# Performance work log

Measured on AMD Instinct MI355X. Metric: run time of the kernel, lower is better.

## Reference

```python
import jax, jax.numpy as jnp
import numpy as np

B, T_IN, T_OUT = 512, 256, 128
V, N, EH, DH, SD = 256, 1024, 64, 128, 32


def _lstm_scan(gx_seq, W_hh, h0, c0):
    """gx_seq: (T, B, 4H) precomputed input-side gates (incl. bias).
    PyTorch LSTMCell gate order: i, f, g, o."""
    def step(carry, gx):
        h, c = carry
        g = gx + h @ W_hh.T                       # (B, 4H)
        i, f, gg, o = jnp.split(g, 4, axis=-1)
        c2 = jax.nn.sigmoid(f) * c + jax.nn.sigmoid(i) * jnp.tanh(gg)
        h2 = jax.nn.sigmoid(o) * jnp.tanh(c2)
        return (h2, c2), h2
    (hT, cT), hs = jax.lax.scan(step, (h0, c0), gx_seq)
    return hT, hs


def _forward(inp_onehot, zia, tgt, fortza,
             enc_Wih, enc_Whh, enc_b, sg_W, sg_b,
             Wc_W, Wc_b, dec_Wih, dec_Whh, dec_b, out_W, out_b):
    Bb = inp_onehot.shape[0]
    dt = inp_onehot.dtype
    # ---- encoder: input projection hoisted out of the recurrence ----
    # enc_in = concat([x_t, zia]); zia is constant over t, so its gate
    # contribution is computed once (same math as the per-step cat+GEMM).
    Wx, Wz = enc_Wih[:, :V], enc_Wih[:, V:]          # (4EH,V), (4EH,N)
    gx_const = zia @ Wz.T + enc_b                    # (B, 4EH)
    gx_enc = jnp.einsum('btv,gv->tbg', inp_onehot, Wx) + gx_const[None]
    h0 = jnp.zeros((Bb, EH), dt)
    h_enc, _ = _lstm_scan(gx_enc, enc_Whh, h0, h0)   # (B, EH)
    # ---- soul update ----
    sg = jnp.concatenate([h_enc, fortza], axis=-1) @ sg_W.T + sg_b
    gate = jax.nn.sigmoid(sg[:, :SD])
    update = jnp.tanh(sg[:, SD:])
    fortza_new = gate * fortza + (1.0 - gate) * update
    # ---- decoder init ----
    dh0 = jnp.tanh(jnp.concatenate([h_enc, zia], axis=-1) @ Wc_W.T + Wc_b)
    dc0 = jnp.zeros_like(dh0)
    # ---- decoder recurrence ----
    gx_dec = jnp.einsum('btv,gv->tbg', tgt, dec_Wih) + dec_b
    _, dhs = _lstm_scan(gx_dec, dec_Whh, dh0, dc0)   # (T_out, B, DH)
    # ---- output projection: split cat([dh, fortza_new]) @ W.T ----
    Wd, Wf = out_W[:, :DH], out_W[:, DH:]
    logits = (jnp.einsum('tbh,vh->btv', dhs, Wd)
              + (fortza_new @ Wf.T)[:, None, :] + out_b)
    return logits, fortza_new


def setup_inputs() -> dict:
    key = jax.random.key(0)
    ks = jax.random.split(key, 20)
    f32 = jnp.float32
    def nrm(k, shape, s=0.05):
        return jax.random.normal(k, shape, f32) * s
    inp_idx = jax.random.randint(ks[0], (B, T_IN), 0, V)
    tgt_idx = jax.random.randint(ks[1], (B, T_OUT), 0, V)
    return {
        'inp_onehot': jax.nn.one_hot(inp_idx, V, dtype=f32),
        'zia': jax.random.uniform(ks[2], (B, N), f32),
        'tgt': jax.nn.one_hot(tgt_idx, V, dtype=f32),
        'fortza': nrm(ks[3], (B, SD), 0.5),
        'enc_Wih': nrm(ks[4], (4 * EH, V + N)),
        'enc_Whh': nrm(ks[5], (4 * EH, EH)),
        'enc_b': nrm(ks[6], (4 * EH,)),
        'sg_W': nrm(ks[7], (2 * SD, EH + SD)),
        'sg_b': nrm(ks[8], (2 * SD,)),
        'Wc_W': nrm(ks[9], (DH, EH + N)),
        'Wc_b': nrm(ks[10], (DH,)),
        'dec_Wih': nrm(ks[11], (4 * DH, V)),
        'dec_Whh': nrm(ks[12], (4 * DH, DH)),
        'dec_b': nrm(ks[13], (4 * DH,)),
        'out_W': nrm(ks[14], (V, DH + SD)),
        'out_b': nrm(ks[15], (V,)),
    }


def reference(inp_onehot, zia, tgt, fortza,
              enc_Wih, enc_Whh, enc_b, sg_W, sg_b,
              Wc_W, Wc_b, dec_Wih, dec_Whh, dec_b, out_W, out_b):
    return _forward(inp_onehot, zia, tgt, fortza,
                    enc_Wih, enc_Whh, enc_b, sg_W, sg_b,
                    Wc_W, Wc_b, dec_Wih, dec_Whh, dec_b, out_W, out_b)
```

## Files before the change

kernel.cpp:

```cpp
#include <hip/hip_runtime.h>
#include <hip/hip_bf16.h>

#define BATCH 512
#define TIN   256
#define TOUT  128
#define VOC   256
#define NZ    1024
#define EHID  64
#define DHID  128
#define SDIM  32

typedef __attribute__((ext_vector_type(8))) short bf16x8;
typedef __attribute__((ext_vector_type(4))) float f32x4;

__device__ __forceinline__ float bf2f(unsigned short u) {
  return __uint_as_float(((unsigned)u) << 16);
}
__device__ __forceinline__ unsigned short f2bf(float f) {
  unsigned u = __float_as_uint(f);
  u = u + 0x7FFFu + ((u >> 16) & 1u);
  return (unsigned short)(u >> 16);
}
__device__ __forceinline__ float sigf(float x) { return 1.0f / (1.0f + __expf(-x)); }
__device__ __forceinline__ float tanh_(float x) { return 1.0f - 2.0f / (1.0f + __expf(2.0f * x)); }

__device__ __forceinline__ bf16x8 pack8(float4 a, float4 b) {
  bf16x8 r;
  r[0] = (short)f2bf(a.x); r[1] = (short)f2bf(a.y);
  r[2] = (short)f2bf(a.z); r[3] = (short)f2bf(a.w);
  r[4] = (short)f2bf(b.x); r[5] = (short)f2bf(b.y);
  r[6] = (short)f2bf(b.z); r[7] = (short)f2bf(b.w);
  return r;
}

__global__ void k_prep(const float* __restrict__ enc_Wih, const float* __restrict__ enc_b,
                       const float* __restrict__ dec_Wih, const float* __restrict__ dec_b,
                       const float* __restrict__ out_W,
                       float* __restrict__ WxT, float* __restrict__ WdecT,
                       float* __restrict__ WdT) {
  int blk = blockIdx.x, tid = threadIdx.x;
  if (blk < 256) {
    if (tid < 256)
      WxT[blk * 256 + tid] = enc_Wih[(size_t)tid * (VOC + NZ) + blk] + enc_b[tid];
  } else if (blk < 512) {
    int v = blk - 256;
    WdecT[v * 512 + tid] = dec_Wih[(size_t)tid * VOC + v] + dec_b[tid];
  } else {
    int k = blk - 512;
    if (tid < 256)
      WdT[k * 256 + tid] = out_W[(size_t)tid * (DHID + SDIM) + k];
  }
}

__global__ void k_findidx(const float* __restrict__ src, int n_pos,
                          int* __restrict__ out) {
  int pos = blockIdx.x * 4 + (threadIdx.x >> 6);
  int lane = threadIdx.x & 63;
  if (pos >= n_pos) return;
  float4 v = ((const float4*)src)[(size_t)pos * 64 + lane];
  int comp = v.x > 0.5f ? 0 : (v.y > 0.5f ? 1 : (v.z > 0.5f ? 2 : 3));
  bool hit = (v.x > 0.5f) || (v.y > 0.5f) || (v.z > 0.5f) || (v.w > 0.5f);
  int cand = hit ? lane * 4 + comp : (1 << 30);
#pragma unroll
  for (int off = 32; off > 0; off >>= 1) {
    int o = __shfl_xor(cand, off);
    cand = cand < o ? cand : o;
  }
  if (lane == 0) out[pos] = cand < VOC ? cand : VOC - 1;
}

__global__ __launch_bounds__(256) void k_gx_const(
    const float* __restrict__ zia, const float* __restrict__ enc_Wih,
    float* __restrict__ gxc) {
  __shared__ float zs[NZ];
  int b = blockIdx.x, g = threadIdx.x;
  ((float4*)zs)[g] = ((const float4*)(zia + (size_t)b * NZ))[g];
  __syncthreads();
  float acc = 0.0f;
  const float4* wr = (const float4*)(enc_Wih + (size_t)g * (VOC + NZ) + VOC);
  const float4* z4 = (const float4*)zs;
#pragma unroll 8
  for (int k4 = 0; k4 < NZ / 4; ++k4) {
    float4 w = wr[k4], z = z4[k4];
    acc += w.x * z.x + w.y * z.y + w.z * z.z + w.w * z.w;
  }
  gxc[b * 256 + g] = acc;
}

#define ESTR 72
__global__ __launch_bounds__(256) void k_enc_scan_mfma(
    const float* __restrict__ enc_Whh, const float* __restrict__ WxT,
    const float* __restrict__ gxc, const int* __restrict__ enc_idx,
    float* __restrict__ h_enc) {
  __shared__ unsigned short hA[2][16 * ESTR];
  __shared__ int idx_s[4][TIN];
  int b0 = blockIdx.x * 4;
  int tid = threadIdx.x;
  int w = tid >> 6, lane = tid & 63, n = lane & 15, quad = lane >> 4;
  int j0 = w * 16, j = j0 + n;

  bf16x8 Bf[4][2];
#pragma unroll
  for (int ty = 0; ty < 4; ++ty)
#pragma unroll
    for (int kb = 0; kb < 2; ++kb) {
      const float* src = enc_Whh + (size_t)(ty * 64 + j0 + n) * EHID + kb * 32 + quad * 8;
      float4 x = *(const float4*)src, y = *(const float4*)(src + 4);
      Bf[ty][kb] = pack8(x, y);
    }
  for (int i = tid; i < 16 * ESTR; i += 256) { hA[0][i] = 0; hA[1][i] = 0; }
  for (int i = tid; i < 4 * TIN; i += 256)
    idx_s[i >> 8][i & 255] = enc_idx[(size_t)(b0 + (i >> 8)) * TIN + (i & 255)];
  float gc[4];
#pragma unroll
  for (int ty = 0; ty < 4; ++ty) gc[ty] = gxc[(size_t)(b0 + quad) * 256 + ty * 64 + j];
  __syncthreads();

  float gx[4];
  {
    int id0 = idx_s[quad][0];
#pragma unroll
    for (int ty = 0; ty < 4; ++ty) gx[ty] = WxT[(size_t)id0 * 256 + ty * 64 + j];
  }
  float c0 = 0.0f, h = 0.0f;
  for (int t = 0; t < TIN; ++t) {
    const unsigned short* cur = hA[t & 1];
    bf16x8 a[2];
#pragma unroll
    for (int kb = 0; kb < 2; ++kb)
      a[kb] = *(const bf16x8*)(cur + n * ESTR + kb * 32 + quad * 8);
    float gxn[4];
    int tn = (t + 1 < TIN) ? t + 1 : t;
    int idn = idx_s[quad][tn];
#pragma unroll
    for (int ty = 0; ty < 4; ++ty) gxn[ty] = WxT[(size_t)idn * 256 + ty * 64 + j];
    f32x4 acc[4];
#pragma unroll
    for (int ty = 0; ty < 4; ++ty) {
      f32x4 z; z[0] = gx[ty] + gc[ty]; z[1] = 0.f; z[2] = 0.f; z[3] = 0.f;
#pragma unroll
      for (int kb = 0; kb < 2; ++kb)
        z = __builtin_amdgcn_mfma_f32_16x16x32_bf16(a[kb], Bf[ty][kb], z, 0, 0, 0);
      acc[ty] = z;
    }
    float gi = acc[0][0], gf = acc[1][0], gg = acc[2][0], go = acc[3][0];
    c0 = sigf(gf) * c0 + sigf(gi) * tanh_(gg);
    h = sigf(go) * tanh_(c0);
    hA[(t + 1) & 1][(quad * 4) * ESTR + j] = f2bf(h);
    gx[0] = gxn[0]; gx[1] = gxn[1]; gx[2] = gxn[2]; gx[3] = gxn[3];
    __syncthreads();
  }
  h_enc[(size_t)(b0 + quad) * EHID + j] = h;
}

__global__ __launch_bounds__(256) void k_sg_fortza(
    const float* __restrict__ h_enc, const float* __restrict__ fortza,
    const float* __restrict__ sg_W, const float* __restrict__ sg_b,
    const float* __restrict__ out_W, const float* __restrict__ out_b,
    float* __restrict__ out_fortza, float* __restrict__ fout) {
  __shared__ float hf[EHID], fz[SDIM], sg_s[2 * SDIM], fn[SDIM];
  int b = blockIdx.x, tid = threadIdx.x;
  if (tid < EHID) hf[tid] = h_enc[b * EHID + tid];
  if (tid >= EHID && tid < EHID + SDIM)
    fz[tid - EHID] = fortza[(size_t)b * SDIM + (tid - EHID)];
  __syncthreads();
  if (tid < 2 * SDIM) {
    float acc = sg_b[tid];
    const float* row = sg_W + (size_t)tid * (EHID + SDIM);
    for (int k = 0; k < EHID; ++k) acc += hf[k] * row[k];
    for (int j = 0; j < SDIM; ++j) acc += fz[j] * row[EHID + j];
    sg_s[tid] = acc;
  }
  __syncthreads();
  if (tid < SDIM) {
    float gate = sigf(sg_s[tid]);
    float upd = tanh_(sg_s[SDIM + tid]);
    float v = gate * fz[tid] + (1.0f - gate) * upd;
    fn[tid] = v;
    out_fortza[(size_t)b * SDIM + tid] = v;
  }
  __syncthreads();
  {
    float acc = out_b[tid];
    const float* row = out_W + (size_t)tid * (DHID + SDIM) + DHID;
    for (int j = 0; j < SDIM; ++j) acc += fn[j] * row[j];
    fout[b * VOC + tid] = acc;
  }
}

__global__ __launch_bounds__(128) void k_dh0(
    const float* __restrict__ h_enc, const float* __restrict__ zia,
    const float* __restrict__ Wc_W, const float* __restrict__ Wc_b,
    float* __restrict__ dh0) {
  __shared__ float xs[EHID + NZ];
  int b = blockIdx.x, v = threadIdx.x;
  if (v < EHID) xs[v] = h_enc[b * EHID + v];
  for (int i = v; i < NZ / 4; i += 128)
    ((float4*)(xs + EHID))[i] = ((const float4*)(zia + (size_t)b * NZ))[i];
  __syncthreads();
  float acc = Wc_b[v];
  const float4* wr = (const float4*)(Wc_W + (size_t)v * (EHID + NZ));
  const float4* x4 = (const float4*)xs;
#pragma unroll 8
  for (int k4 = 0; k4 < (EHID + NZ) / 4; ++k4) {
    float4 w = wr[k4], x = x4[k4];
    acc += w.x * x.x + w.y * x.y + w.z * x.z + w.w * x.w;
  }
  dh0[b * DHID + v] = tanh_(acc);
}

#define DSTR 136
__global__ __launch_bounds__(512) void k_dec_scan_mfma(
    const float* __restrict__ dec_Whh, const float* __restrict__ WdecT,
    const int* __restrict__ dec_idx, const float* __restrict__ dh0,
    unsigned short* __restrict__ dhs) {
  __shared__ unsigned short hA[2][16 * DSTR];
  __shared__ int idx_s[4][TOUT];
  int b0 = blockIdx.x * 4;
  int tid = threadIdx.x;
  int w = tid >> 6, lane = tid & 63, n = lane & 15, quad = lane >> 4;
  int j0 = w * 16, j = j0 + n;

  bf16x8 Bf[4][4];
#pragma unroll
  for (int ty = 0; ty < 4; ++ty)
#pragma unroll
    for (int kb = 0; kb < 4; ++kb) {
      const float* src = dec_Whh + (size_t)(ty * 128 + j0 + n) * DHID + kb * 32 + quad * 8;
      float4 x = *(const float4*)src, y = *(const float4*)(src + 4);
      Bf[ty][kb] = pack8(x, y);
    }
  for (int i = tid; i < 16 * DSTR; i += 512) {
    int m = i / DSTR, k = i - m * DSTR;
    float v = (k < DHID && (m & 3) == 0) ? dh0[(size_t)(b0 + (m >> 2)) * DHID + k] : 0.0f;
    hA[0][i] = f2bf(v);
    hA[1][i] = 0;
  }
  for (int i = tid; i < 4 * TOUT; i += 512)
    idx_s[i >> 7][i & 127] = dec_idx[(size_t)(b0 + (i >> 7)) * TOUT + (i & 127)];
  __syncthreads();

  float gx[4];
  {
    int id0 = idx_s[quad][0];
#pragma unroll
    for (int ty = 0; ty < 4; ++ty) gx[ty] = WdecT[(size_t)id0 * 512 + ty * 128 + j];
  }
  float c0 = 0.0f;
  for (int t = 0; t < TOUT; ++t) {
    const unsigned short* cur = hA[t & 1];
    bf16x8 a[4];
#pragma unroll
    for (int kb = 0; kb < 4; ++kb)
      a[kb] = *(const bf16x8*)(cur + n * DSTR + kb * 32 + quad * 8);
    float gxn[4];
    int tn = (t + 1 < TOUT) ? t + 1 : t;
    int idn = idx_s[quad][tn];
#pragma unroll
    for (int ty = 0; ty < 4; ++ty) gxn[ty] = WdecT[(size_t)idn * 512 + ty * 128 + j];
    f32x4 acc[4];
#pragma unroll
    for (int ty = 0; ty < 4; ++ty) {
      f32x4 z; z[0] = gx[ty]; z[1] = 0.f; z[2] = 0.f; z[3] = 0.f;
#pragma unroll
      for (int kb = 0; kb < 4; ++kb)
        z = __builtin_amdgcn_mfma_f32_16x16x32_bf16(a[kb], Bf[ty][kb], z, 0, 0, 0);
      acc[ty] = z;
    }
    float gi = acc[0][0], gf = acc[1][0], gg = acc[2][0], go = acc[3][0];
    c0 = sigf(gf) * c0 + sigf(gi) * tanh_(gg);
    float h = sigf(go) * tanh_(c0);
    unsigned short hb = f2bf(h);
    hA[(t + 1) & 1][(quad * 4) * DSTR + j] = hb;
    dhs[((size_t)t * BATCH + b0 + quad) * DHID + j] = hb;
    gx[0] = gxn[0]; gx[1] = gxn[1]; gx[2] = gxn[2]; gx[3] = gxn[3];
    __syncthreads();
  }
}

__global__ __launch_bounds__(256) void k_logits(const unsigned short* __restrict__ dhs,
                                                const float* __restrict__ WdT,
                                                const float* __restrict__ fout,
                                                float* __restrict__ out) {
  __shared__ float s[DHID * 64];
  int r0 = blockIdx.x * 64;
  int t = r0 / BATCH;
  int b0 = r0 % BATCH;
  int tid = threadIdx.x;
  for (int i = tid; i < 64 * DHID; i += 256) {
    int m = i >> 7;
    int k = i & 127;
    s[k * 64 + m] = bf2f(dhs[(size_t)(r0 + m) * DHID + k]);
  }
  __syncthreads();
  int v4 = tid & 63;
  int mg = tid >> 6;
  float4 acc[16];
#pragma unroll
  for (int m = 0; m < 16; ++m) acc[m] = make_float4(0.f, 0.f, 0.f, 0.f);
  for (int k = 0; k < DHID; ++k) {
    float4 wv = ((const float4*)(WdT + k * 256))[v4];
    const float4* sk = (const float4*)(s + k * 64 + mg * 16);
#pragma unroll
    for (int j = 0; j < 4; ++j) {
      float4 h4 = sk[j];
      acc[j * 4 + 0].x += h4.x * wv.x; acc[j * 4 + 0].y += h4.x * wv.y;
      acc[j * 4 + 0].z += h4.x * wv.z; acc[j * 4 + 0].w += h4.x * wv.w;
      acc[j * 4 + 1].x += h4.y * wv.x; acc[j * 4 + 1].y += h4.y * wv.y;
      acc[j * 4 + 1].z += h4.y * wv.z; acc[j * 4 + 1].w += h4.y * wv.w;
      acc[j * 4 + 2].x += h4.z * wv.x; acc[j * 4 + 2].y += h4.z * wv.y;
      acc[j * 4 + 2].z += h4.z * wv.z; acc[j * 4 + 2].w += h4.z * wv.w;
      acc[j * 4 + 3].x += h4.w * wv.x; acc[j * 4 + 3].y += h4.w * wv.y;
      acc[j * 4 + 3].z += h4.w * wv.z; acc[j * 4 + 3].w += h4.w * wv.w;
    }
  }
#pragma unroll
  for (int m = 0; m < 16; ++m) {
    int bb = b0 + mg * 16 + m;
    float4 fo = ((const float4*)(fout + bb * VOC))[v4];
    float4 r;
    r.x = acc[m].x + fo.x;
    r.y = acc[m].y + fo.y;
    r.z = acc[m].z + fo.z;
    r.w = acc[m].w + fo.w;
    ((float4*)(out + ((size_t)bb * TOUT + t) * VOC))[v4] = r;
  }
}

extern "C" void kernel_launch(void* const* d_in, const int* in_sizes, int n_in,
                              void* d_out, int out_size, void* d_ws, size_t ws_size,
                              hipStream_t stream) {
  const float* inp_onehot = (const float*)d_in[0];
  const float* zia     = (const float*)d_in[1];
  const float* tgt     = (const float*)d_in[2];
  const float* fortza  = (const float*)d_in[3];
  const float* enc_Wih = (const float*)d_in[4];
  const float* enc_Whh = (const float*)d_in[5];
  const float* enc_b   = (const float*)d_in[6];
  const float* sg_W    = (const float*)d_in[7];
  const float* sg_b    = (const float*)d_in[8];
  const float* Wc_W    = (const float*)d_in[9];
  const float* Wc_b    = (const float*)d_in[10];
  const float* dec_Wih = (const float*)d_in[11];
  const float* dec_Whh = (const float*)d_in[12];
  const float* dec_b   = (const float*)d_in[13];
  const float* out_W   = (const float*)d_in[14];
  const float* out_b   = (const float*)d_in[15];
  float* out = (float*)d_out;

  float* ws = (float*)d_ws;
  int* enc_idx  = (int*)d_ws;
  int* dec_idx  = enc_idx + BATCH * TIN;
  float* WxT    = ws + 196608;
  float* WdecT  = ws + 262144;
  float* WdT    = ws + 393216;
  float* gxc    = ws + 425984;
  float* h_enc  = ws + 557056;
  float* dh0    = ws + 589824;
  float* fout   = ws + 655360;
  unsigned short* dhs = (unsigned short*)(ws + 786432);

  k_prep<<<640, 512, 0, stream>>>(enc_Wih, enc_b, dec_Wih, dec_b, out_W, WxT, WdecT, WdT);
  k_findidx<<<BATCH * TIN / 4, 256, 0, stream>>>(inp_onehot, BATCH * TIN, enc_idx);
  k_findidx<<<BATCH * TOUT / 4, 256, 0, stream>>>(tgt, BATCH * TOUT, dec_idx);
  k_gx_const<<<BATCH, 256, 0, stream>>>(zia, enc_Wih, gxc);
  k_enc_scan_mfma<<<BATCH / 4, 256, 0, stream>>>(enc_Whh, WxT, gxc, enc_idx, h_enc);
  k_sg_fortza<<<BATCH, 256, 0, stream>>>(h_enc, fortza, sg_W, sg_b, out_W, out_b,
                                         out + (size_t)BATCH * TOUT * VOC, fout);
  k_dh0<<<BATCH, 128, 0, stream>>>(h_enc, zia, Wc_W, Wc_b, dh0);
  k_dec_scan_mfma<<<BATCH / 4, 512, 0, stream>>>(dec_Whh, WdecT, dec_idx, dh0, dhs);
  k_logits<<<TOUT * BATCH / 64, 256, 0, stream>>>(dhs, WdT, fout, out);
}
```

Measured before the change: 629.5 us.

## Merge prep kernels and overlap decoder prep with encoder scan via block-role dispatch

Collapses nine launches into five by giving blocks of one launch different roles. The decoder weight transposes and target index extraction now run as extra blocks alongside the latency-bound encoder scan, so they can use otherwise idle CUs. The zia-side gate GEMM and the decoder init GEMM are rewritten as shared-memory tiled 32x32 GEMMs, and the weight transposes go through an LDS tile for coalesced access. The cost is a larger, more divergent kernel with heavier resource use, which could reduce occupancy of the scan blocks or delay their scheduling behind the auxiliary blocks.

Result: faster. 568.6 us (-9.7%).

```diff
diff --git a/kernel.cpp b/kernel.cpp
--- a/kernel.cpp
+++ b/kernel.cpp
@@ -33,30 +33,9 @@
   return r;
 }
 
-__global__ void k_prep(const float* __restrict__ enc_Wih, const float* __restrict__ enc_b,
-                       const float* __restrict__ dec_Wih, const float* __restrict__ dec_b,
-                       const float* __restrict__ out_W,
-                       float* __restrict__ WxT, float* __restrict__ WdecT,
-                       float* __restrict__ WdT) {
-  int blk = blockIdx.x, tid = threadIdx.x;
-  if (blk < 256) {
-    if (tid < 256)
-      WxT[blk * 256 + tid] = enc_Wih[(size_t)tid * (VOC + NZ) + blk] + enc_b[tid];
-  } else if (blk < 512) {
-    int v = blk - 256;
-    WdecT[v * 512 + tid] = dec_Wih[(size_t)tid * VOC + v] + dec_b[tid];
-  } else {
-    int k = blk - 512;
-    if (tid < 256)
-      WdT[k * 256 + tid] = out_W[(size_t)tid * (DHID + SDIM) + k];
-  }
-}
-
-__global__ void k_findidx(const float* __restrict__ src, int n_pos,
-                          int* __restrict__ out) {
-  int pos = blockIdx.x * 4 + (threadIdx.x >> 6);
-  int lane = threadIdx.x & 63;
-  if (pos >= n_pos) return;
+__device__ __forceinline__ void dev_findidx(const float* __restrict__ src,
+                                            int pos, int lane,
+                                            int* __restrict__ out) {
   float4 v = ((const float4*)src)[(size_t)pos * 64 + lane];
   int comp = v.x > 0.5f ? 0 : (v.y > 0.5f ? 1 : (v.z > 0.5f ? 2 : 3));
   bool hit = (v.x > 0.5f) || (v.y > 0.5f) || (v.z > 0.5f) || (v.w > 0.5f);
@@ -69,148 +48,218 @@
   if (lane == 0) out[pos] = cand < VOC ? cand : VOC - 1;
 }
 
-__global__ __launch_bounds__(256) void k_gx_const(
-    const float* __restrict__ zia, const float* __restrict__ enc_Wih,
-    float* __restrict__ gxc) {
-  __shared__ float zs[NZ];
-  int b = blockIdx.x, g = threadIdx.x;
-  ((float4*)zs)[g] = ((const float4*)(zia + (size_t)b * NZ))[g];
-  __syncthreads();
-  float acc = 0.0f;
-  const float4* wr = (const float4*)(enc_Wih + (size_t)g * (VOC + NZ) + VOC);
-  const float4* z4 = (const float4*)zs;
-#pragma unroll 8
-  for (int k4 = 0; k4 < NZ / 4; ++k4) {
-    float4 w = wr[k4], z = z4[k4];
-    acc += w.x * z.x + w.y * z.y + w.z * z.z + w.w * z.w;
-  }
-  gxc[b * 256 + g] = acc;
+__global__ __launch_bounds__(256) void k_pre(
+    const float* __restrict__ enc_Wih, const float* __restrict__ enc_b,
+    const float* __restrict__ inp_onehot, const float* __restrict__ zia,
+    float* __restrict__ WxT, float* __restrict__ gxc, int* __restrict__ enc_idx) {
+  int blk = blockIdx.x, tid = threadIdx.x;
+  if (blk < 64) {
+    __shared__ float T[32][36];
+    int r = tid >> 3, c = (tid & 7) * 4;
+    int g0 = (blk >> 3) * 32, v0 = (blk & 7) * 32;
+    float4 v = *(const float4*)(enc_Wih + (size_t)(g0 + r) * (VOC + NZ) + v0 + c);
+    float bias = enc_b[g0 + r];
+    T[c + 0][r] = v.x + bias; T[c + 1][r] = v.y + bias;
+    T[c + 2][r] = v.z + bias; T[c + 3][r] = v.w + bias;
+    __syncthreads();
+    *(float4*)(WxT + (size_t)(v0 + r) * 256 + g0 + c) = *(const float4*)&T[r][c];
+  } else if (blk < 192) {
+    __shared__ float As[32][36], Bs[32][36];
+    int q = blk - 64;
+    int b0 = (q & 15) * 32, g0 = (q >> 4) * 32;
+    int ldr = tid >> 3, ldc = (tid & 7) * 4;
+    int tx = tid & 15, ty = tid >> 4;
+    float a00 = 0.f, a01 = 0.f, a10 = 0.f, a11 = 0.f;
+    for (int kc = 0; kc < NZ; kc += 32) {
+      float4 av = *(const float4*)(zia + (size_t)(b0 + ldr) * NZ + kc + ldc);
+      float4 bv = *(const float4*)(enc_Wih + (size_t)(g0 + ldr) * (VOC + NZ) + VOC + kc + ldc);
+      __syncthreads();
+      As[ldc + 0][ldr] = av.x; As[ldc + 1][ldr] = av.y;
+      As[ldc + 2][ldr] = av.z; As[ldc + 3][ldr] = av.w;
+      Bs[ldc + 0][ldr] = bv.x; Bs[ldc + 1][ldr] = bv.y;
+      Bs[ldc + 2][ldr] = bv.z; Bs[ldc + 3][ldr] = bv.w;
+      __syncthreads();
+#pragma unroll
+      for (int k = 0; k < 32; ++k) {
+        float x0 = As[k][tx * 2], x1 = As[k][tx * 2 + 1];
+        float y0 = Bs[k][ty * 2], y1 = Bs[k][ty * 2 + 1];
+        a00 += x0 * y0; a01 += x0 * y1; a10 += x1 * y0; a11 += x1 * y1;
+      }
+    }
+    float* o = gxc + (size_t)(b0 + tx * 2) * 256 + g0 + ty * 2;
+    o[0] = a00; o[1] = a01; o[256] = a10; o[257] = a11;
+  } else {
+    int pos = (blk - 192) * 4 + (tid >> 6);
+    if (pos < BATCH * TIN) dev_findidx(inp_onehot, pos, tid & 63, enc_idx);
+  }
 }
 
 #define ESTR 72
-__global__ __launch_bounds__(256) void k_enc_scan_mfma(
+__global__ __launch_bounds__(256) void k_enc_fused(
     const float* __restrict__ enc_Whh, const float* __restrict__ WxT,
     const float* __restrict__ gxc, const int* __restrict__ enc_idx,
-    float* __restrict__ h_enc) {
-  __shared__ unsigned short hA[2][16 * ESTR];
-  __shared__ int idx_s[4][TIN];
-  int b0 = blockIdx.x * 4;
-  int tid = threadIdx.x;
-  int w = tid >> 6, lane = tid & 63, n = lane & 15, quad = lane >> 4;
-  int j0 = w * 16, j = j0 + n;
-
-  bf16x8 Bf[4][2];
-#pragma unroll
-  for (int ty = 0; ty < 4; ++ty)
-#pragma unroll
-    for (int kb = 0; kb < 2; ++kb) {
-      const float* src = enc_Whh + (size_t)(ty * 64 + j0 + n) * EHID + kb * 32 + quad * 8;
-      float4 x = *(const float4*)src, y = *(const float4*)(src + 4);
-      Bf[ty][kb] = pack8(x, y);
-    }
-  for (int i = tid; i < 16 * ESTR; i += 256) { hA[0][i] = 0; hA[1][i] = 0; }
-  for (int i = tid; i < 4 * TIN; i += 256)
-    idx_s[i >> 8][i & 255] = enc_idx[(size_t)(b0 + (i >> 8)) * TIN + (i & 255)];
-  float gc[4];
-#pragma unroll
-  for (int ty = 0; ty < 4; ++ty) gc[ty] = gxc[(size_t)(b0 + quad) * 256 + ty * 64 + j];
-  __syncthreads();
-
-  float gx[4];
-  {
-    int id0 = idx_s[quad][0];
-#pragma unroll
-    for (int ty = 0; ty < 4; ++ty) gx[ty] = WxT[(size_t)id0 * 256 + ty * 64 + j];
-  }
-  float c0 = 0.0f, h = 0.0f;
-  for (int t = 0; t < TIN; ++t) {
-    const unsigned short* cur = hA[t & 1];
-    bf16x8 a[2];
-#pragma unroll
-    for (int kb = 0; kb < 2; ++kb)
-      a[kb] = *(const bf16x8*)(cur + n * ESTR + kb * 32 + quad * 8);
-    float gxn[4];
-    int tn = (t + 1 < TIN) ? t + 1 : t;
-    int idn = idx_s[quad][tn];
-#pragma unroll
-    for (int ty = 0; ty < 4; ++ty) gxn[ty] = WxT[(size_t)idn * 256 + ty * 64 + j];
-    f32x4 acc[4];
-#pragma unroll
-    for (int ty = 0; ty < 4; ++ty) {
-      f32x4 z; z[0] = gx[ty] + gc[ty]; z[1] = 0.f; z[2] = 0.f; z[3] = 0.f;
+    float* __restrict__ h_enc,
+    const float* __restrict__ dec_Wih, const float* __restrict__ dec_b,
+    const float* __restrict__ out_W, const float* __restrict__ tgt,
+    float* __restrict__ WdecT, float* __restrict__ WdT, int* __restrict__ dec_idx) {
+  int blk = blockIdx.x, tid = threadIdx.x;
+  if (blk < 128) {
+    __shared__ unsigned short hA[2][16 * ESTR];
+    __shared__ int idx_s[4][TIN];
+    int b0 = blk * 4;
+    int w = tid >> 6, lane = tid & 63, n = lane & 15, quad = lane >> 4;
+    int j = w * 16 + n;
+
+    bf16x8 Bf[4][2];
+#pragma unroll
+    for (int ty = 0; ty < 4; ++ty)
+#pragma unroll
+      for (int kb = 0; kb < 2; ++kb) {
+        const float* s = enc_Whh + (size_t)(ty * 64 + j) * EHID + kb * 32 + quad * 8;
+        Bf[ty][kb] = pack8(*(const float4*)s, *(const float4*)(s + 4));
+      }
+    for (int i = tid; i < 16 * ESTR; i += 256) { hA[0][i] = 0; hA[1][i] = 0; }
+    for (int i = tid; i < 4 * TIN; i += 256)
+      idx_s[i >> 8][i & 255] = enc_idx[(size_t)(b0 + (i >> 8)) * TIN + (i & 255)];
+    float gc[4];
+#pragma unroll
+    for (int ty = 0; ty < 4; ++ty) gc[ty] = gxc[(size_t)(b0 + quad) * 256 + ty * 64 + j];
+    __syncthreads();
+
+    float gx[4];
+    {
+      int id0 = idx_s[quad][0];
+#pragma unroll
+      for (int ty = 0; ty < 4; ++ty) gx[ty] = WxT[(size_t)id0 * 256 + ty * 64 + j];
+    }
+    float c0 = 0.0f, h = 0.0f;
+    for (int t = 0; t < TIN; ++t) {
+      const unsigned short* cur = hA[t & 1];
+      bf16x8 a[2];
 #pragma unroll
       for (int kb = 0; kb < 2; ++kb)
-        z = __builtin_amdgcn_mfma_f32_16x16x32_bf16(a[kb], Bf[ty][kb], z, 0, 0, 0);
-      acc[ty] = z;
-    }
-    float gi = acc[0][0], gf = acc[1][0], gg = acc[2][0], go = acc[3][0];
-    c0 = sigf(gf) * c0 + sigf(gi) * tanh_(gg);
-    h = sigf(go) * tanh_(c0);
-    hA[(t + 1) & 1][(quad * 4) * ESTR + j] = f2bf(h);
-    gx[0] = gxn[0]; gx[1] = gxn[1]; gx[2] = gxn[2]; gx[3] = gxn[3];
-    __syncthreads();
-  }
-  h_enc[(size_t)(b0 + quad) * EHID + j] = h;
-}
-
-__global__ __launch_bounds__(256) void k_sg_fortza(
+        a[kb] = *(const bf16x8*)(cur + n * ESTR + kb * 32 + quad * 8);
+      float gxn[4];
+      int tn = (t + 1 < TIN) ? t + 1 : t;
+      int idn = idx_s[quad][tn];
+#pragma unroll
+      for (int ty = 0; ty < 4; ++ty) gxn[ty] = WxT[(size_t)idn * 256 + ty * 64 + j];
+      f32x4 acc[4];
+#pragma unroll
+      for (int ty = 0; ty < 4; ++ty) {
+        f32x4 z; z[0] = gx[ty] + gc[ty]; z[1] = 0.f; z[2] = 0.f; z[3] = 0.f;
+        z = __builtin_amdgcn_mfma_f32_16x16x32_bf16(a[0], Bf[ty][0], z, 0, 0, 0);
+        z = __builtin_amdgcn_mfma_f32_16x16x32_bf16(a[1], Bf[ty][1], z, 0, 0, 0);
+        acc[ty] = z;
+      }
+      float gi = acc[0][0], gf = acc[1][0], gg = acc[2][0], go = acc[3][0];
+      c0 = sigf(gf) * c0 + sigf(gi) * tanh_(gg);
+      h = sigf(go) * tanh_(c0);
+      hA[(t + 1) & 1][(quad * 4) * ESTR + j] = f2bf(h);
+      gx[0] = gxn[0]; gx[1] = gxn[1]; gx[2] = gxn[2]; gx[3] = gxn[3];
+      __syncthreads();
+    }
+    h_enc[(size_t)(b0 + quad) * EHID + j] = h;
+  } else if (blk < 256) {
+    __shared__ float T[32][36];
+    int q = blk - 128;
+    int r = tid >> 3, c = (tid & 7) * 4;
+    int g0 = (q >> 3) * 32, v0 = (q & 7) * 32;
+    float4 v = *(const float4*)(dec_Wih + (size_t)(g0 + r) * VOC + v0 + c);
+    float bias = dec_b[g0 + r];
+    T[c + 0][r] = v.x + bias; T[c + 1][r] = v.y + bias;
+    T[c + 2][r] = v.z + bias; T[c + 3][r] = v.w + bias;
+    __syncthreads();
+    *(float4*)(WdecT + (size_t)(v0 + r) * 512 + g0 + c) = *(const float4*)&T[r][c];
+  } else if (blk < 288) {
+    __shared__ float T2[32][36];
+    int q = blk - 256;
+    int r = tid >> 3, c = (tid & 7) * 4;
+    int v0 = (q >> 2) * 32, k0 = (q & 3) * 32;
+    float4 v = *(const float4*)(out_W + (size_t)(v0 + r) * (DHID + SDIM) + k0 + c);
+    T2[c + 0][r] = v.x; T2[c + 1][r] = v.y; T2[c + 2][r] = v.z; T2[c + 3][r] = v.w;
+    __syncthreads();
+    *(float4*)(WdT + (size_t)(k0 + r) * 256 + v0 + c) = *(const float4*)&T2[r][c];
+  } else {
+    int pos = (blk - 288) * 4 + (tid >> 6);
+    if (pos < BATCH * TOUT) dev_findidx(tgt, pos, tid & 63, dec_idx);
+  }
+}
+
+__global__ __launch_bounds__(256) void k_mid(
     const float* __restrict__ h_enc, const float* __restrict__ fortza,
     const float* __restrict__ sg_W, const float* __restrict__ sg_b,
     const float* __restrict__ out_W, const float* __restrict__ out_b,
-    float* __restrict__ out_fortza, float* __restrict__ fout) {
-  __shared__ float hf[EHID], fz[SDIM], sg_s[2 * SDIM], fn[SDIM];
-  int b = blockIdx.x, tid = threadIdx.x;
-  if (tid < EHID) hf[tid] = h_enc[b * EHID + tid];
-  if (tid >= EHID && tid < EHID + SDIM)
-    fz[tid - EHID] = fortza[(size_t)b * SDIM + (tid - EHID)];
-  __syncthreads();
-  if (tid < 2 * SDIM) {
-    float acc = sg_b[tid];
-    const float* row = sg_W + (size_t)tid * (EHID + SDIM);
-    for (int k = 0; k < EHID; ++k) acc += hf[k] * row[k];
-    for (int j = 0; j < SDIM; ++j) acc += fz[j] * row[EHID + j];
-    sg_s[tid] = acc;
-  }
-  __syncthreads();
-  if (tid < SDIM) {
-    float gate = sigf(sg_s[tid]);
-    float upd = tanh_(sg_s[SDIM + tid]);
-    float v = gate * fz[tid] + (1.0f - gate) * upd;
-    fn[tid] = v;
-    out_fortza[(size_t)b * SDIM + tid] = v;
-  }
-  __syncthreads();
-  {
-    float acc = out_b[tid];
-    const float* row = out_W + (size_t)tid * (DHID + SDIM) + DHID;
-    for (int j = 0; j < SDIM; ++j) acc += fn[j] * row[j];
-    fout[b * VOC + tid] = acc;
-  }
-}
-
-__global__ __launch_bounds__(128) void k_dh0(
-    const float* __restrict__ h_enc, const float* __restrict__ zia,
-    const float* __restrict__ Wc_W, const float* __restrict__ Wc_b,
+    const float* __restrict__ zia, const float* __restrict__ Wc_W,
+    const float* __restrict__ Wc_b,
+    float* __restrict__ out_fortza, float* __restrict__ fout,
     float* __restrict__ dh0) {
-  __shared__ float xs[EHID + NZ];
-  int b = blockIdx.x, v = threadIdx.x;
-  if (v < EHID) xs[v] = h_enc[b * EHID + v];
-  for (int i = v; i < NZ / 4; i += 128)
-    ((float4*)(xs + EHID))[i] = ((const float4*)(zia + (size_t)b * NZ))[i];
-  __syncthreads();
-  float acc = Wc_b[v];
-  const float4* wr = (const float4*)(Wc_W + (size_t)v * (EHID + NZ));
-  const float4* x4 = (const float4*)xs;
-#pragma unroll 8
-  for (int k4 = 0; k4 < (EHID + NZ) / 4; ++k4) {
-    float4 w = wr[k4], x = x4[k4];
-    acc += w.x * x.x + w.y * x.y + w.z * x.z + w.w * x.w;
-  }
-  dh0[b * DHID + v] = tanh_(acc);
+  int blk = blockIdx.x, tid = threadIdx.x;
+  if (blk < 512) {
+    __shared__ float hf[EHID], fz[SDIM], sg_s[2 * SDIM], fn[SDIM];
+    int b = blk;
+    if (tid < EHID) hf[tid] = h_enc[b * EHID + tid];
+    if (tid >= EHID && tid < EHID + SDIM)
+      fz[tid - EHID] = fortza[(size_t)b * SDIM + (tid - EHID)];
+    __syncthreads();
+    if (tid < 2 * SDIM) {
+      float acc = sg_b[tid];
+      const float* row = sg_W + (size_t)tid * (EHID + SDIM);
+      for (int k = 0; k < EHID; ++k) acc += hf[k] * row[k];
+      for (int jj = 0; jj < SDIM; ++jj) acc += fz[jj] * row[EHID + jj];
+      sg_s[tid] = acc;
+    }
+    __syncthreads();
+    if (tid < SDIM) {
+      float gate = sigf(sg_s[tid]);
+      float upd = tanh_(sg_s[SDIM + tid]);
+      float v = gate * fz[tid] + (1.0f - gate) * upd;
+      fn[tid] = v;
+      out_fortza[(size_t)b * SDIM + tid] = v;
+    }
+    __syncthreads();
+    {
+      float acc = out_b[tid];
+      const float* row = out_W + (size_t)tid * (DHID + SDIM) + DHID;
+      for (int jj = 0; jj < SDIM; ++jj) acc += fn[jj] * row[jj];
+      fout[b * VOC + tid] = acc;
+    }
+  } else {
+    __shared__ float As[32][36], Bs[32][36];
+    int q = blk - 512;
+    int b0 = (q & 15) * 32, v0 = (q >> 4) * 32;
+    int ldr = tid >> 3, ldc = (tid & 7) * 4;
+    int tx = tid & 15, ty = tid >> 4;
+    float a00 = 0.f, a01 = 0.f, a10 = 0.f, a11 = 0.f;
+    for (int kc = 0; kc < EHID + NZ; kc += 32) {
+      float4 av;
+      if (kc < EHID)
+        av = *(const float4*)(h_enc + (size_t)(b0 + ldr) * EHID + kc + ldc);
+      else
+        av = *(const float4*)(zia + (size_t)(b0 + ldr) * NZ + (kc - EHID) + ldc);
+      float4 bv = *(const float4*)(Wc_W + (size_t)(v0 + ldr) * (EHID + NZ) + kc + ldc);
+      __syncthreads();
+      As[ldc + 0][ldr] = av.x; As[ldc + 1][ldr] = av.y;
+      As[ldc + 2][ldr] = av.z; As[ldc + 3][ldr] = av.w;
+      Bs[ldc + 0][ldr] = bv.x; Bs[ldc + 1][ldr] = bv.y;
+      Bs[ldc + 2][ldr] = bv.z; Bs[ldc + 3][ldr] = bv.w;
+      __syncthreads();
+#pragma unroll
+      for (int k = 0; k < 32; ++k) {
+        float x0 = As[k][tx * 2], x1 = As[k][tx * 2 + 1];
+        float y0 = Bs[k][ty * 2], y1 = Bs[k][ty * 2 + 1];
+        a00 += x0 * y0; a01 += x0 * y1; a10 += x1 * y0; a11 += x1 * y1;
+      }
+    }
+    float bb0 = Wc_b[v0 + ty * 2], bb1 = Wc_b[v0 + ty * 2 + 1];
+    float* o = dh0 + (size_t)(b0 + tx * 2) * DHID + v0 + ty * 2;
+    o[0] = tanh_(a00 + bb0); o[1] = tanh_(a01 + bb1);
+    o[DHID] = tanh_(a10 + bb0); o[DHID + 1] = tanh_(a11 + bb1);
+  }
 }
 
 #define DSTR 136
-__global__ __launch_bounds__(512) void k_dec_scan_mfma(
+__global__ __launch_bounds__(512) void k_dec_scan(
     const float* __restrict__ dec_Whh, const float* __restrict__ WdecT,
     const int* __restrict__ dec_idx, const float* __restrict__ dh0,
     unsigned short* __restrict__ dhs) {
@@ -227,8 +276,7 @@
 #pragma unroll
     for (int kb = 0; kb < 4; ++kb) {
       const float* src = dec_Whh + (size_t)(ty * 128 + j0 + n) * DHID + kb * 32 + quad * 8;
-      float4 x = *(const float4*)src, y = *(const float4*)(src + 4);
-      Bf[ty][kb] = pack8(x, y);
+      Bf[ty][kb] = pack8(*(const float4*)src, *(const float4*)(src + 4));
     }
   for (int i = tid; i < 16 * DSTR; i += 512) {
     int m = i / DSTR, k = i - m * DSTR;
@@ -302,16 +350,16 @@
     float4 wv = ((const float4*)(WdT + k * 256))[v4];
     const float4* sk = (const float4*)(s + k * 64 + mg * 16);
 #pragma unroll
-    for (int j = 0; j < 4; ++j) {
-      float4 h4 = sk[j];
-      acc[j * 4 + 0].x += h4.x * wv.x; acc[j * 4 + 0].y += h4.x * wv.y;
-      acc[j * 4 + 0].z += h4.x * wv.z; acc[j * 4 + 0].w += h4.x * wv.w;
-      acc[j * 4 + 1].x += h4.y * wv.x; acc[j * 4 + 1].y += h4.y * wv.y;
-      acc[j * 4 + 1].z += h4.y * wv.z; acc[j * 4 + 1].w += h4.y * wv.w;
-      acc[j * 4 + 2].x += h4.z * wv.x; acc[j * 4 + 2].y += h4.z * wv.y;
-      acc[j * 4 + 2].z += h4.z * wv.z; acc[j * 4 + 2].w += h4.z * wv.w;
-      acc[j * 4 + 3].x += h4.w * wv.x; acc[j * 4 + 3].y += h4.w * wv.y;
-      acc[j * 4 + 3].z += h4.w * wv.z; acc[j * 4 + 3].w += h4.w * wv.w;
+    for (int jj = 0; jj < 4; ++jj) {
+      float4 h4 = sk[jj];
+      acc[jj * 4 + 0].x += h4.x * wv.x; acc[jj * 4 + 0].y += h4.x * wv.y;
+      acc[jj * 4 + 0].z += h4.x * wv.z; acc[jj * 4 + 0].w += h4.x * wv.w;
+      acc[jj * 4 + 1].x += h4.y * wv.x; acc[jj * 4 + 1].y += h4.y * wv.y;
+      acc[jj * 4 + 1].z += h4.y * wv.z; acc[jj * 4 + 1].w += h4.y * wv.w;
+      acc[jj * 4 + 2].x += h4.z * wv.x; acc[jj * 4 + 2].y += h4.z * wv.y;
+      acc[jj * 4 + 2].z += h4.z * wv.z; acc[jj * 4 + 2].w += h4.z * wv.w;
+      acc[jj * 4 + 3].x += h4.w * wv.x; acc[jj * 4 + 3].y += h4.w * wv.y;
+      acc[jj * 4 + 3].z += h4.w * wv.z; acc[jj * 4 + 3].w += h4.w * wv.w;
     }
   }
 #pragma unroll
@@ -360,14 +408,14 @@
   float* fout   = ws + 655360;
   unsigned short* dhs = (unsigned short*)(ws + 786432);
 
-  k_prep<<<640, 512, 0, stream>>>(enc_Wih, enc_b, dec_Wih, dec_b, out_W, WxT, WdecT, WdT);
-  k_findidx<<<BATCH * TIN / 4, 256, 0, stream>>>(inp_onehot, BATCH * TIN, enc_idx);
-  k_findidx<<<BATCH * TOUT / 4, 256, 0, stream>>>(tgt, BATCH * TOUT, dec_idx);
-  k_gx_const<<<BATCH, 256, 0, stream>>>(zia, enc_Wih, gxc);
-  k_enc_scan_mfma<<<BATCH / 4, 256, 0, stream>>>(enc_Whh, WxT, gxc, enc_idx, h_enc);
-  k_sg_fortza<<<BATCH, 256, 0, stream>>>(h_enc, fortza, sg_W, sg_b, out_W, out_b,
-                                         out + (size_t)BATCH * TOUT * VOC, fout);
-  k_dh0<<<BATCH, 128, 0, stream>>>(h_enc, zia, Wc_W, Wc_b, dh0);
-  k_dec_scan_mfma<<<BATCH / 4, 512, 0, stream>>>(dec_Whh, WdecT, dec_idx, dh0, dhs);
+  k_pre<<<192 + BATCH * TIN / 4, 256, 0, stream>>>(
+      enc_Wih, enc_b, inp_onehot, zia, WxT, gxc, enc_idx);
+  k_enc_fused<<<288 + BATCH * TOUT / 4, 256, 0, stream>>>(
+      enc_Whh, WxT, gxc, enc_idx, h_enc,
+      dec_Wih, dec_b, out_W, tgt, WdecT, WdT, dec_idx);
+  k_mid<<<576, 256, 0, stream>>>(h_enc, fortza, sg_W, sg_b, out_W, out_b,
+                                 zia, Wc_W, Wc_b,
+                                 out + (size_t)BATCH * TOUT * VOC, fout, dh0);
+  k_dec_scan<<<BATCH / 4, 512, 0, stream>>>(dec_Whh, WdecT, dec_idx, dh0, dhs);
   k_logits<<<TOUT * BATCH / 64, 256, 0, stream>>>(dhs, WdT, fout, out);
 }
```
